# Kernel tuning notes

Hardware: AMD Instinct MI355X
Metric: run time of the kernel (lower is better)

Reference implementation:

```python
import jax, jax.numpy as jnp
import numpy as np

N_GROUPS = 4
N_CODES = 160
EMBED_DIM = 512
GROUP_DIM = EMBED_DIM // N_GROUPS  # 128


def setup_inputs() -> dict:
    key = jax.random.key(0)
    k1, k2 = jax.random.split(key)
    B, T = 16, 4096
    xin = jax.random.normal(k1, (B, EMBED_DIM, T), dtype=jnp.float32)
    # matches nn.Embedding init: uniform(-1/n_e, 1/n_e)
    codebook = jax.random.uniform(k2, (N_GROUPS, N_CODES, GROUP_DIM), dtype=jnp.float32,
                                  minval=-1.0 / N_CODES, maxval=1.0 / N_CODES)
    return {"xin": xin, "codebook": codebook}


def _quantize(xin, codebook):
    B, C, T = xin.shape
    x_btc = jnp.transpose(xin, (0, 2, 1))            # [B, T, C]
    x = x_btc.reshape(-1, N_GROUPS, GROUP_DIM)       # [N, G, D]
    # squared euclidean distance per group: [N, G, K]
    d = (jnp.sum(x ** 2, axis=-1, keepdims=True)
         + jnp.sum(codebook ** 2, axis=-1)[None, :, :]
         - 2.0 * jnp.einsum('ngd,gkd->ngk', x, codebook))
    idx = jnp.argmin(d, axis=-1)                     # [N, G] int
    # gather codewords: [N, G, D]
    z_q = jnp.take_along_axis(codebook[None], idx[:, :, None, None], axis=2)[:, :, 0, :]
    z_q = z_q.reshape(B, T, C)                       # [B, T, C]
    return x_btc, z_q, idx.reshape(B, T, N_GROUPS)


def reference(xin, codebook):
    B, C, T = xin.shape
    x_btc, z_q, codes = _quantize(xin, codebook)
    sg = jax.lax.stop_gradient
    loss = 0.25 * jnp.mean((sg(z_q) - x_btc) ** 2) + jnp.mean((z_q - sg(x_btc)) ** 2)
    z_q_st = x_btc + sg(z_q - x_btc)                 # straight-through
    z_q_out = jnp.transpose(z_q_st, (0, 2, 1))       # [B, C, T]
    codes_out = jnp.transpose(codes, (0, 2, 1))      # [B, G, T]
    return z_q_out, loss, codes_out
```

## Files before the change

### kernel.cpp

```cpp
#include <hip/hip_runtime.h>
#include <stdint.h>

#define NG 4
#define NK 160
#define GD 128
#define ED 512
#define BB 16
#define TT 4096
static constexpr size_t ZSZ = (size_t)BB * ED * TT;

typedef float f32x4 __attribute__((ext_vector_type(4)));


__global__ void prep_kernel(const float* __restrict__ cb, float* __restrict__ sc,
                            float* __restrict__ ct) {
  int i = blockIdx.x * 256 + threadIdx.x;
  int g = i / (GD * NK), r = i % (GD * NK), d = r / NK, k = r % NK;
  ct[i] = cb[((size_t)g * NK + k) * GD + d];
  if (i < NG * NK) {
    const float* c = cb + (size_t)i * GD;
    float s = 0.f;
    for (int dd = 0; dd < GD; ++dd) s = fmaf(c[dd], c[dd], s);
    sc[i] = s;
  }
}

__global__ __launch_bounds__(512) void vq_kernel(const float* __restrict__ xin,
                                                 const float* __restrict__ cb,
                                                 const float* __restrict__ sc,
                                                 const float* __restrict__ ct,
                                                 float* __restrict__ out,
                                                 float* __restrict__ bsum) {
  __shared__ float bestW[8 * 256];
  __shared__ int bikW[8 * 256];
  __shared__ float wred[4];

  const int tid = (int)threadIdx.x;
  const int w = tid >> 6;
  const int l = tid & 63;
  const int g = (int)(blockIdx.x >> 8);
  const int tb = (int)(blockIdx.x & 255);
  const int b = tb >> 4;
  const int t0 = (tb & 15) << 8;

  const float* xp = xin + ((size_t)(b * ED + g * GD)) * TT + t0 + l * 4;
  const float* ctg = ct + (size_t)g * GD * NK;
  const int kbase = __builtin_amdgcn_readfirstlane(w) * 20;

  float acc[4][20];
#pragma unroll
  for (int i = 0; i < 4; ++i)
#pragma unroll
    for (int j = 0; j < 20; ++j) acc[i][j] = 0.f;
  float sxa[4] = {0.f, 0.f, 0.f, 0.f};

#pragma unroll 2
  for (int dd = 0; dd < GD; ++dd) {
    const f32x4 xv = *(const f32x4*)(xp + (size_t)dd * TT);
    const float* cw = ctg + (size_t)dd * NK + kbase;
    const f32x4 c0 = *(const f32x4*)&cw[0];
    const f32x4 c1 = *(const f32x4*)&cw[4];
    const f32x4 c2 = *(const f32x4*)&cw[8];
    const f32x4 c3 = *(const f32x4*)&cw[12];
    const f32x4 c4 = *(const f32x4*)&cw[16];
#pragma unroll
    for (int i = 0; i < 4; ++i) sxa[i] = fmaf(xv[i], xv[i], sxa[i]);
#pragma unroll
    for (int i = 0; i < 4; ++i) {
      const float xf = xv[i];
#pragma unroll
      for (int e = 0; e < 4; ++e) {
        acc[i][e] = fmaf(xf, c0[e], acc[i][e]);
        acc[i][4 + e] = fmaf(xf, c1[e], acc[i][4 + e]);
        acc[i][8 + e] = fmaf(xf, c2[e], acc[i][8 + e]);
        acc[i][12 + e] = fmaf(xf, c3[e], acc[i][12 + e]);
        acc[i][16 + e] = fmaf(xf, c4[e], acc[i][16 + e]);
      }
    }
  }

  const float* scw = sc + g * NK + kbase;
  float best[4] = {3.4e38f, 3.4e38f, 3.4e38f, 3.4e38f};
  int bik[4] = {0, 0, 0, 0};
#pragma unroll
  for (int j = 0; j < 20; ++j) {
    const float scv = scw[j];
#pragma unroll
    for (int i = 0; i < 4; ++i) {
      const float dv = (sxa[i] + scv) - 2.0f * acc[i][j];
      if (dv < best[i]) { best[i] = dv; bik[i] = kbase + j; }
    }
  }

  *(f32x4*)&bestW[w * 256 + l * 4] = (f32x4){best[0], best[1], best[2], best[3]};
#pragma unroll
  for (int i = 0; i < 4; ++i) bikW[w * 256 + l * 4 + i] = bik[i];
  __syncthreads();

  if (tid < 256) {
    float bf = bestW[tid];
    int kf = bikW[tid];
#pragma unroll
    for (int ww = 1; ww < 8; ++ww) {
      float bw = bestW[ww * 256 + tid];
      int kw = bikW[ww * 256 + tid];
      if (bw < bf) { bf = bw; kf = kw; }
    }

    out[ZSZ + 1 + ((size_t)(b * NG + g)) * TT + t0 + tid] = (float)kf;

    const f32x4* cw = (const f32x4*)(cb + ((size_t)g * NK + kf) * GD);
    float* zbase = out + ((size_t)(b * ED + g * GD)) * TT + t0 + tid;
#pragma unroll 4
    for (int d4 = 0; d4 < 32; ++d4) {
      f32x4 v = cw[d4];
      zbase[(size_t)(4 * d4 + 0) * TT] = v[0];
      zbase[(size_t)(4 * d4 + 1) * TT] = v[1];
      zbase[(size_t)(4 * d4 + 2) * TT] = v[2];
      zbase[(size_t)(4 * d4 + 3) * TT] = v[3];
    }

    float s = bf;
#pragma unroll
    for (int off = 32; off > 0; off >>= 1) s += __shfl_down(s, off, 64);
    if (l == 0) wred[w] = s;
  }
  __syncthreads();
  if (tid == 0)
    bsum[blockIdx.x] = ((wred[0] + wred[1]) + wred[2]) + wred[3];
}

__global__ __launch_bounds__(64) void loss_kernel(const float* __restrict__ bsum,
                                                  float* __restrict__ out) {
  float s = 0.f;
  for (int j = 0; j < 16; ++j) s += bsum[threadIdx.x + 64 * j];
#pragma unroll
  for (int off = 32; off > 0; off >>= 1) s += __shfl_down(s, off, 64);
  if (threadIdx.x == 0) out[ZSZ] = 1.25f * s / (float)ZSZ;
}

extern "C" void kernel_launch(void* const* d_in, const int* in_sizes, int n_in,
                              void* d_out, int out_size, void* d_ws, size_t ws_size,
                              hipStream_t stream) {
  const float* xin = (const float*)d_in[0];
  const float* cb  = (const float*)d_in[1];
  float* out  = (float*)d_out;
  float* bsum = (float*)d_ws;
  float* sc   = (float*)d_ws + 1024;
  float* ct   = (float*)d_ws + 2048;

  prep_kernel<<<320, 256, 0, stream>>>(cb, sc, ct);
  vq_kernel<<<1024, 512, 0, stream>>>(xin, cb, sc, ct, out, bsum);
  loss_kernel<<<1, 64, 0, stream>>>(bsum, out);
}
```

Measured before the change: 146.7 us.

## Software-pipeline distance loop loads and split codeword writeback across all threads

The dot-product loop becomes manually software-pipelined. Eight x rows are held in registers and double-buffered codebook fragments are prefetched one step ahead, so global load latency overlaps with FMAs. The z_q writeback, previously done by only 256 of 512 threads, is now spread over all 512 threads, each writing half of the 128 dims, through a shared-memory index buffer. Costs are higher register pressure from 8 extra f32x4 x-registers and 10 codebook registers, which could hurt occupancy or cause spills.

```diff
diff --git a/kernel.cpp b/kernel.cpp
--- a/kernel.cpp
+++ b/kernel.cpp
@@ -25,6 +25,34 @@
   }
 }
 
+#define XLOAD(R_, DD) R_ = *(const f32x4*)(xp + (size_t)(DD) * TT)
+
+#define CLOAD(P_, DD)                                                      \
+  do {                                                                     \
+    const float* cwp_ = ctg + (size_t)(DD) * NK + kbase;                   \
+    P_##0 = *(const f32x4*)&cwp_[0];                                       \
+    P_##1 = *(const f32x4*)&cwp_[4];                                       \
+    P_##2 = *(const f32x4*)&cwp_[8];                                       \
+    P_##3 = *(const f32x4*)&cwp_[12];                                      \
+    P_##4 = *(const f32x4*)&cwp_[16];                                      \
+  } while (0)
+
+#define COMP(XV, P_)                                                       \
+  do {                                                                     \
+    _Pragma("unroll") for (int i_ = 0; i_ < 4; ++i_)                       \
+        sxa[i_] = fmaf((XV)[i_], (XV)[i_], sxa[i_]);                       \
+    _Pragma("unroll") for (int i_ = 0; i_ < 4; ++i_) {                     \
+      const float xf_ = (XV)[i_];                                          \
+      _Pragma("unroll") for (int e_ = 0; e_ < 4; ++e_) {                   \
+        acc[i_][e_] = fmaf(xf_, (P_##0)[e_], acc[i_][e_]);                 \
+        acc[i_][4 + e_] = fmaf(xf_, (P_##1)[e_], acc[i_][4 + e_]);         \
+        acc[i_][8 + e_] = fmaf(xf_, (P_##2)[e_], acc[i_][8 + e_]);         \
+        acc[i_][12 + e_] = fmaf(xf_, (P_##3)[e_], acc[i_][12 + e_]);       \
+        acc[i_][16 + e_] = fmaf(xf_, (P_##4)[e_], acc[i_][16 + e_]);       \
+      }                                                                    \
+    }                                                                      \
+  } while (0)
+
 __global__ __launch_bounds__(512) void vq_kernel(const float* __restrict__ xin,
                                                  const float* __restrict__ cb,
                                                  const float* __restrict__ sc,
@@ -33,6 +61,7 @@
                                                  float* __restrict__ bsum) {
   __shared__ float bestW[8 * 256];
   __shared__ int bikW[8 * 256];
+  __shared__ int kfS[256];
   __shared__ float wred[4];
 
   const int tid = (int)threadIdx.x;
@@ -54,30 +83,32 @@
     for (int j = 0; j < 20; ++j) acc[i][j] = 0.f;
   float sxa[4] = {0.f, 0.f, 0.f, 0.f};
 
-#pragma unroll 2
-  for (int dd = 0; dd < GD; ++dd) {
-    const f32x4 xv = *(const f32x4*)(xp + (size_t)dd * TT);
-    const float* cw = ctg + (size_t)dd * NK + kbase;
-    const f32x4 c0 = *(const f32x4*)&cw[0];
-    const f32x4 c1 = *(const f32x4*)&cw[4];
-    const f32x4 c2 = *(const f32x4*)&cw[8];
-    const f32x4 c3 = *(const f32x4*)&cw[12];
-    const f32x4 c4 = *(const f32x4*)&cw[16];
-#pragma unroll
-    for (int i = 0; i < 4; ++i) sxa[i] = fmaf(xv[i], xv[i], sxa[i]);
-#pragma unroll
-    for (int i = 0; i < 4; ++i) {
-      const float xf = xv[i];
-#pragma unroll
-      for (int e = 0; e < 4; ++e) {
-        acc[i][e] = fmaf(xf, c0[e], acc[i][e]);
-        acc[i][4 + e] = fmaf(xf, c1[e], acc[i][4 + e]);
-        acc[i][8 + e] = fmaf(xf, c2[e], acc[i][8 + e]);
-        acc[i][12 + e] = fmaf(xf, c3[e], acc[i][12 + e]);
-        acc[i][16 + e] = fmaf(xf, c4[e], acc[i][16 + e]);
-      }
-    }
+  f32x4 x0, x1, x2, x3, x4, x5, x6, x7;
+  f32x4 cA0, cA1, cA2, cA3, cA4, cB0, cB1, cB2, cB3, cB4;
+
+  XLOAD(x0, 0); XLOAD(x1, 1); XLOAD(x2, 2); XLOAD(x3, 3);
+  XLOAD(x4, 4); XLOAD(x5, 5); XLOAD(x6, 6); XLOAD(x7, 7);
+  CLOAD(cA, 0);
+
+#pragma unroll 1
+  for (int dd8 = 0; dd8 < 120; dd8 += 8) {
+    CLOAD(cB, dd8 + 1); COMP(x0, cA); XLOAD(x0, dd8 + 8);
+    CLOAD(cA, dd8 + 2); COMP(x1, cB); XLOAD(x1, dd8 + 9);
+    CLOAD(cB, dd8 + 3); COMP(x2, cA); XLOAD(x2, dd8 + 10);
+    CLOAD(cA, dd8 + 4); COMP(x3, cB); XLOAD(x3, dd8 + 11);
+    CLOAD(cB, dd8 + 5); COMP(x4, cA); XLOAD(x4, dd8 + 12);
+    CLOAD(cA, dd8 + 6); COMP(x5, cB); XLOAD(x5, dd8 + 13);
+    CLOAD(cB, dd8 + 7); COMP(x6, cA); XLOAD(x6, dd8 + 14);
+    CLOAD(cA, dd8 + 8); COMP(x7, cB); XLOAD(x7, dd8 + 15);
   }
+  CLOAD(cB, 121); COMP(x0, cA);
+  CLOAD(cA, 122); COMP(x1, cB);
+  CLOAD(cB, 123); COMP(x2, cA);
+  CLOAD(cA, 124); COMP(x3, cB);
+  CLOAD(cB, 125); COMP(x4, cA);
+  CLOAD(cA, 126); COMP(x5, cB);
+  CLOAD(cB, 127); COMP(x6, cA);
+  COMP(x7, cB);
 
   const float* scw = sc + g * NK + kbase;
   float best[4] = {3.4e38f, 3.4e38f, 3.4e38f, 3.4e38f};
@@ -106,19 +137,9 @@
       int kw = bikW[ww * 256 + tid];
       if (bw < bf) { bf = bw; kf = kw; }
     }
+    kfS[tid] = kf;
 
     out[ZSZ + 1 + ((size_t)(b * NG + g)) * TT + t0 + tid] = (float)kf;
-
-    const f32x4* cw = (const f32x4*)(cb + ((size_t)g * NK + kf) * GD);
-    float* zbase = out + ((size_t)(b * ED + g * GD)) * TT + t0 + tid;
-#pragma unroll 4
-    for (int d4 = 0; d4 < 32; ++d4) {
-      f32x4 v = cw[d4];
-      zbase[(size_t)(4 * d4 + 0) * TT] = v[0];
-      zbase[(size_t)(4 * d4 + 1) * TT] = v[1];
-      zbase[(size_t)(4 * d4 + 2) * TT] = v[2];
-      zbase[(size_t)(4 * d4 + 3) * TT] = v[3];
-    }
 
     float s = bf;
 #pragma unroll
@@ -126,6 +147,24 @@
     if (l == 0) wred[w] = s;
   }
   __syncthreads();
+
+  {
+    const int tok = tid & 255;
+    const int half = tid >> 8;
+    const int kf = kfS[tok];
+    const f32x4* cw = (const f32x4*)(cb + ((size_t)g * NK + kf) * GD) + half * 16;
+    float* zbase = out + ((size_t)(b * ED + g * GD) + (size_t)half * 64) * TT
+                   + t0 + tok;
+#pragma unroll 4
+    for (int d4 = 0; d4 < 16; ++d4) {
+      f32x4 v = cw[d4];
+      zbase[(size_t)(4 * d4 + 0) * TT] = v[0];
+      zbase[(size_t)(4 * d4 + 1) * TT] = v[1];
+      zbase[(size_t)(4 * d4 + 2) * TT] = v[2];
+      zbase[(size_t)(4 * d4 + 3) * TT] = v[3];
+    }
+  }
+
   if (tid == 0)
     bsum[blockIdx.x] = ((wred[0] + wred[1]) + wred[2]) + wred[3];
 }
```

After: 214.6 us. +46.3%, slower.
